# Optimization experiments

Measured on AMD Instinct MI355X. Metric: run time of the kernel, lower is better.

The kernel has to match this reference:

```python
import jax, jax.numpy as jnp
import numpy as np

D_MODEL = 1024


def setup_inputs() -> dict:
    key = jax.random.key(0)
    kx, kq, kk, kv = jax.random.split(key, 4)
    x = jax.random.normal(kx, (4, 2048, D_MODEL), dtype=jnp.float32)
    s = 1.0 / np.sqrt(D_MODEL)
    # torch nn.Linear weight is [out, in]; y = x @ W.T
    Wq = jax.random.normal(kq, (D_MODEL, D_MODEL), dtype=jnp.float32) * s
    Wk = jax.random.normal(kk, (D_MODEL, D_MODEL), dtype=jnp.float32) * s
    Wv = jax.random.normal(kv, (D_MODEL, D_MODEL), dtype=jnp.float32) * s
    return {"x": x, "Wq": Wq, "Wk": Wk, "Wv": Wv}


def reference(x, Wq, Wk, Wv):
    # Linear projections (no bias): [b, s, d]
    Q = jnp.einsum("bsd,ed->bse", x, Wq)
    K = jnp.einsum("bsd,ed->bse", x, Wk)
    V = jnp.einsum("bsd,ed->bse", x, Wv)
    d_k = Q.shape[-1]
    scores = jnp.einsum("bqd,bkd->bqk", Q, K) / jnp.sqrt(jnp.asarray(d_k, Q.dtype))
    weights = jax.nn.softmax(scores, axis=-1)
    return jnp.einsum("bqk,bkd->bqd", weights, V)
```

## Files before the change

### kernel.cpp

```cpp
#include <hip/hip_runtime.h>
#include <hip/hip_bf16.h>

using bf16 = __hip_bfloat16;
typedef __attribute__((ext_vector_type(8))) short short8;
typedef __attribute__((ext_vector_type(4))) float f32x4;

__global__ __launch_bounds__(256) void cast_f32_to_bf16(const float* __restrict__ in,
                                                        bf16* __restrict__ out) {
  const int i = (blockIdx.x * 256 + threadIdx.x) * 4;
  const float4 f = *(const float4*)(in + i);
  bf16 h[4];
  h[0] = __float2bfloat16(f.x);
  h[1] = __float2bfloat16(f.y);
  h[2] = __float2bfloat16(f.z);
  h[3] = __float2bfloat16(f.w);
  *(uint2*)(out + i) = *(const uint2*)h;
}

template <class Epi>
__device__ __forceinline__ void gemm128_nt(const bf16* __restrict__ A, const bf16* __restrict__ B,
                                           int lda, int ldb, int K, Epi epi) {
  __shared__ char smem[36864];
  bf16* As = (bf16*)smem;
  bf16* Bs = (bf16*)(smem + 8192);
  const int t = threadIdx.x;
  const int lane = t & 63;
  const int wave = t >> 6;
  const int wm = (wave >> 1) * 64;
  const int wn = (wave & 1) * 64;
  const int m0 = blockIdx.y * 128;
  const int n0 = blockIdx.x * 128;

  f32x4 acc[4][4];
#pragma unroll
  for (int i = 0; i < 4; ++i)
#pragma unroll
    for (int j = 0; j < 4; ++j)
#pragma unroll
      for (int r = 0; r < 4; ++r) acc[i][j][r] = 0.f;

  const int r0 = t >> 2;
  const int fsw = (r0 + (r0 >> 2)) & 3;
  const int cglob = ((t & 3) ^ fsw) << 3;
  const bf16* gA0 = A + (size_t)(m0 + r0) * lda + cglob;
  const bf16* gB0 = B + (size_t)(n0 + r0) * ldb + cglob;
  const bf16* gA1 = gA0 + (size_t)64 * lda;
  const bf16* gB1 = gB0 + (size_t)64 * ldb;
  bf16* lA = As + (size_t)wave * 64 * 8;
  bf16* lB = Bs + (size_t)wave * 64 * 8;

  const int fr = lane & 15;
  const int ffr = (fr + (fr >> 2)) & 3;
  const int csw = ((lane >> 4) ^ ffr) << 3;

  for (int k0 = 0; k0 < K; k0 += 32) {
    __builtin_amdgcn_global_load_lds((const __attribute__((address_space(1))) unsigned int*)(gA0 + k0),
                                     (__attribute__((address_space(3))) unsigned int*)lA, 16, 0, 0);
    __builtin_amdgcn_global_load_lds((const __attribute__((address_space(1))) unsigned int*)(gB0 + k0),
                                     (__attribute__((address_space(3))) unsigned int*)lB, 16, 0, 0);
    __builtin_amdgcn_global_load_lds((const __attribute__((address_space(1))) unsigned int*)(gA1 + k0),
                                     (__attribute__((address_space(3))) unsigned int*)(lA + 2048), 16, 0, 0);
    __builtin_amdgcn_global_load_lds((const __attribute__((address_space(1))) unsigned int*)(gB1 + k0),
                                     (__attribute__((address_space(3))) unsigned int*)(lB + 2048), 16, 0, 0);
    __syncthreads();

    short8 af[4], bfr[4];
#pragma unroll
    for (int mt = 0; mt < 4; ++mt)
      af[mt] = *(const short8*)(As + (wm + mt * 16 + fr) * 32 + csw);
#pragma unroll
    for (int nt = 0; nt < 4; ++nt)
      bfr[nt] = *(const short8*)(Bs + (wn + nt * 16 + fr) * 32 + csw);
#pragma unroll
    for (int mt = 0; mt < 4; ++mt)
#pragma unroll
      for (int nt = 0; nt < 4; ++nt)
        acc[mt][nt] = __builtin_amdgcn_mfma_f32_16x16x32_bf16(af[mt], bfr[nt], acc[mt][nt], 0, 0, 0);
    __syncthreads();
  }

  epi(acc, m0, n0, wm, wn, lane, wave, smem);
}

template <class F>
__device__ __forceinline__ void for_each_c(const f32x4 (&acc)[4][4], int m0, int n0, int wm,
                                           int wn, int lane, F f) {
  const int cr = (lane >> 4) * 4;
  const int cc = lane & 15;
#pragma unroll
  for (int mt = 0; mt < 4; ++mt)
#pragma unroll
    for (int nt = 0; nt < 4; ++nt)
#pragma unroll
      for (int r = 0; r < 4; ++r)
        f(m0 + wm + mt * 16 + cr + r, n0 + wn + nt * 16 + cc, acc[mt][nt][r]);
}

__global__ __launch_bounds__(256) void proj_kernel(const bf16* __restrict__ xb,
                                                   const bf16* __restrict__ Wb,
                                                   bf16* __restrict__ Qb, bf16* __restrict__ Kb,
                                                   bf16* __restrict__ Vt) {
  gemm128_nt(xb, Wb, 1024, 1024, 1024,
             [=](const f32x4 (&acc)[4][4], int m0, int n0, int wm, int wn, int lane, int wave,
                 char* smem) {
    if (n0 < 2048) {
      bf16* dst = (n0 < 1024) ? Qb : Kb;
      const int nb = (n0 < 1024) ? n0 : (n0 - 1024);
      for_each_c(acc, m0, nb, wm, wn, lane, [&](int m, int n, float v) {
        dst[(size_t)m * 1024 + n] = __float2bfloat16(v);
      });
    } else {
      bf16* T = (bf16*)smem + wave * 4608;
      const int cr = (lane >> 4) * 4;
      const int cc = lane & 15;
#pragma unroll
      for (int mt = 0; mt < 4; ++mt)
#pragma unroll
        for (int nt = 0; nt < 4; ++nt) {
          bf16 h4[4];
#pragma unroll
          for (int r = 0; r < 4; ++r) h4[r] = __float2bfloat16(acc[mt][nt][r]);
          *(uint2*)(T + (nt * 16 + cc) * 72 + mt * 16 + cr) = *(const uint2*)h4;
        }
      asm volatile("s_waitcnt lgkmcnt(0)" ::: "memory");
      const int mbase = m0 + wm;
      const int bb = mbase >> 11;
      const int sbase = mbase & 2047;
      const int nvbase = n0 - 2048 + wn;
#pragma unroll
      for (int i = 0; i < 8; ++i) {
        const int nl = i * 8 + (lane >> 3);
        const int ml = (lane & 7) * 8;
        const short8 val = *(const short8*)(T + nl * 72 + ml);
        *(short8*)(Vt + ((size_t)bb * 1024 + nvbase + nl) * 2048 + sbase + ml) = val;
      }
    }
  });
}

__global__ __launch_bounds__(256) void qk_exp_kernel(const bf16* __restrict__ Qb,
                                                     const bf16* __restrict__ Kb,
                                                     bf16* __restrict__ E,
                                                     float* __restrict__ Lpart) {
  const int z = blockIdx.z;
  const bf16* A = Qb + (size_t)z * 2048 * 1024;
  const bf16* B = Kb + (size_t)z * 2048 * 1024;
  bf16* Ez = E + (size_t)z * 2048 * 2048;
  float* Lz = Lpart + (size_t)z * 16 * 2048;
  gemm128_nt(A, B, 1024, 1024, 1024,
             [=](const f32x4 (&acc)[4][4], int m0, int n0, int wm, int wn, int lane, int wave,
                 char* smem) {
    float* Lp = (float*)smem;
    const int cr = (lane >> 4) * 4;
    const int cc = lane & 15;
#pragma unroll
    for (int mt = 0; mt < 4; ++mt)
#pragma unroll
      for (int r = 0; r < 4; ++r) {
        const int mr = wm + mt * 16 + cr + r;
        float s = 0.f;
#pragma unroll
        for (int nt = 0; nt < 4; ++nt) {
          const float e = __expf(acc[mt][nt][r] * 0.03125f);
          Ez[(size_t)(m0 + mr) * 2048 + n0 + wn + nt * 16 + cc] = __float2bfloat16(e);
          s += e;
        }
        s += __shfl_xor(s, 1, 64);
        s += __shfl_xor(s, 2, 64);
        s += __shfl_xor(s, 4, 64);
        s += __shfl_xor(s, 8, 64);
        if (cc == 0) Lp[mr * 2 + (wave & 1)] = s;
      }
    __syncthreads();
    const int t = threadIdx.x;
    if (t < 128) Lz[(n0 >> 7) * 2048 + m0 + t] = Lp[t * 2 + 0] + Lp[t * 2 + 1];
  });
}

__global__ __launch_bounds__(256) void reduce_l_kernel(const float* __restrict__ Lpart,
                                                       float* __restrict__ invL) {
  const int i = blockIdx.x * 256 + threadIdx.x;
  const int z = i >> 11, m = i & 2047;
  const float* p = Lpart + (size_t)z * 16 * 2048 + m;
  float s = 0.f;
#pragma unroll
  for (int t = 0; t < 16; ++t) s += p[(size_t)t * 2048];
  invL[i] = 1.f / s;
}

__global__ __launch_bounds__(256) void pv_kernel(const bf16* __restrict__ E,
                                                 const bf16* __restrict__ Vt,
                                                 const float* __restrict__ invL,
                                                 float* __restrict__ out) {
  const int z = blockIdx.z;
  const bf16* A = E + (size_t)z * 2048 * 2048;
  const bf16* B = Vt + (size_t)z * 1024 * 2048;
  const float* ilz = invL + (size_t)z * 2048;
  float* oz = out + (size_t)z * 2048 * 1024;
  gemm128_nt(A, B, 2048, 2048, 2048,
             [=](const f32x4 (&acc)[4][4], int m0, int n0, int wm, int wn, int lane, int wave,
                 char* smem) {
    const int cr = (lane >> 4) * 4;
    const int cc = lane & 15;
#pragma unroll
    for (int mt = 0; mt < 4; ++mt)
#pragma unroll
      for (int r = 0; r < 4; ++r) {
        const int m = m0 + wm + mt * 16 + cr + r;
        const float il = ilz[m];
#pragma unroll
        for (int nt = 0; nt < 4; ++nt)
          oz[(size_t)m * 1024 + n0 + wn + nt * 16 + cc] = acc[mt][nt][r] * il;
      }
  });
}

extern "C" void kernel_launch(void* const* d_in, const int* in_sizes, int n_in,
                              void* d_out, int out_size, void* d_ws, size_t ws_size,
                              hipStream_t stream) {
  const float* x = (const float*)d_in[0];
  const float* Wq = (const float*)d_in[1];
  const float* Wk = (const float*)d_in[2];
  const float* Wv = (const float*)d_in[3];
  float* out = (float*)d_out;

  char* w = (char*)d_ws;
  bf16* xb = (bf16*)w; w += (size_t)8192 * 1024 * 2;
  bf16* Wb = (bf16*)w; w += (size_t)3072 * 1024 * 2;
  bf16* Qb = (bf16*)w; w += (size_t)8192 * 1024 * 2;
  bf16* Kb = (bf16*)w; w += (size_t)8192 * 1024 * 2;
  bf16* Vt = (bf16*)w; w += (size_t)8192 * 1024 * 2;
  bf16* E  = (bf16*)w; w += (size_t)4 * 2048 * 2048 * 2;
  float* Lpart = (float*)w; w += (size_t)4 * 16 * 2048 * 4;
  float* invL  = (float*)w; w += (size_t)4 * 2048 * 4;

  cast_f32_to_bf16<<<8192, 256, 0, stream>>>(x, xb);
  cast_f32_to_bf16<<<1024, 256, 0, stream>>>(Wq, Wb);
  cast_f32_to_bf16<<<1024, 256, 0, stream>>>(Wk, Wb + (size_t)1024 * 1024);
  cast_f32_to_bf16<<<1024, 256, 0, stream>>>(Wv, Wb + (size_t)2048 * 1024);

  proj_kernel<<<dim3(24, 64), 256, 0, stream>>>(xb, Wb, Qb, Kb, Vt);

  qk_exp_kernel<<<dim3(16, 16, 4), 256, 0, stream>>>(Qb, Kb, E, Lpart);
  reduce_l_kernel<<<32, 256, 0, stream>>>(Lpart, invL);

  pv_kernel<<<dim3(8, 16, 4), 256, 0, stream>>>(E, Vt, invL, out);
}
```

Before: 268.6 us.

## Switch GEMM core to 32x32x16 MFMA tiles and merge weight casts

Replaces the 16x16x32 bf16 MFMA tiling (4x4 tiles per wave) with 32x32x16 MFMA (2x2 tiles per wave, two k-substeps per 32-wide LDS tile), and rewrites every epilogue's C-fragment indexing for the new accumulator layout. Each operand fragment now feeds a larger MFMA, so fewer LDS reads are needed per unit of math. The three weight-cast launches are merged into one kernel to cut launch overhead. The epilogue store patterns change: rows are strided by 8 and columns span 32 lanes, which shifts global write coalescing.

```diff
diff --git a/kernel.cpp b/kernel.cpp
--- a/kernel.cpp
+++ b/kernel.cpp
@@ -3,7 +3,7 @@
 
 using bf16 = __hip_bfloat16;
 typedef __attribute__((ext_vector_type(8))) short short8;
-typedef __attribute__((ext_vector_type(4))) float f32x4;
+typedef __attribute__((ext_vector_type(16))) float f32x16;
 
 __global__ __launch_bounds__(256) void cast_f32_to_bf16(const float* __restrict__ in,
                                                         bf16* __restrict__ out) {
@@ -15,6 +15,24 @@
   h[2] = __float2bfloat16(f.z);
   h[3] = __float2bfloat16(f.w);
   *(uint2*)(out + i) = *(const uint2*)h;
+}
+
+__global__ __launch_bounds__(256) void cast_weights(const float* __restrict__ Wq,
+                                                    const float* __restrict__ Wk,
+                                                    const float* __restrict__ Wv,
+                                                    bf16* __restrict__ out) {
+  const int b = blockIdx.x;
+  const float* src = (b < 1024) ? (Wq + (size_t)b * 1024)
+                   : (b < 2048) ? (Wk + (size_t)(b - 1024) * 1024)
+                                : (Wv + (size_t)(b - 2048) * 1024);
+  const int i = threadIdx.x * 4;
+  const float4 f = *(const float4*)(src + i);
+  bf16 h[4];
+  h[0] = __float2bfloat16(f.x);
+  h[1] = __float2bfloat16(f.y);
+  h[2] = __float2bfloat16(f.z);
+  h[3] = __float2bfloat16(f.w);
+  *(uint2*)(out + (size_t)b * 1024 + i) = *(const uint2*)h;
 }
 
 template <class Epi>
@@ -31,13 +49,13 @@
   const int m0 = blockIdx.y * 128;
   const int n0 = blockIdx.x * 128;
 
-  f32x4 acc[4][4];
-#pragma unroll
-  for (int i = 0; i < 4; ++i)
-#pragma unroll
-    for (int j = 0; j < 4; ++j)
-#pragma unroll
-      for (int r = 0; r < 4; ++r) acc[i][j][r] = 0.f;
+  f32x16 acc[2][2];
+#pragma unroll
+  for (int i = 0; i < 2; ++i)
+#pragma unroll
+    for (int j = 0; j < 2; ++j)
+#pragma unroll
+      for (int r = 0; r < 16; ++r) acc[i][j][r] = 0.f;
 
   const int r0 = t >> 2;
   const int fsw = (r0 + (r0 >> 2)) & 3;
@@ -49,9 +67,9 @@
   bf16* lA = As + (size_t)wave * 64 * 8;
   bf16* lB = Bs + (size_t)wave * 64 * 8;
 
-  const int fr = lane & 15;
-  const int ffr = (fr + (fr >> 2)) & 3;
-  const int csw = ((lane >> 4) ^ ffr) << 3;
+  const int rl = lane & 31;
+  const int grp = lane >> 5;
+  const int ffr = (rl + (rl >> 2)) & 3;
 
   for (int k0 = 0; k0 < K; k0 += 32) {
     __builtin_amdgcn_global_load_lds((const __attribute__((address_space(1))) unsigned int*)(gA0 + k0),
@@ -64,36 +82,47 @@
                                      (__attribute__((address_space(3))) unsigned int*)(lB + 2048), 16, 0, 0);
     __syncthreads();
 
-    short8 af[4], bfr[4];
-#pragma unroll
-    for (int mt = 0; mt < 4; ++mt)
-      af[mt] = *(const short8*)(As + (wm + mt * 16 + fr) * 32 + csw);
-#pragma unroll
-    for (int nt = 0; nt < 4; ++nt)
-      bfr[nt] = *(const short8*)(Bs + (wn + nt * 16 + fr) * 32 + csw);
-#pragma unroll
-    for (int mt = 0; mt < 4; ++mt)
-#pragma unroll
-      for (int nt = 0; nt < 4; ++nt)
-        acc[mt][nt] = __builtin_amdgcn_mfma_f32_16x16x32_bf16(af[mt], bfr[nt], acc[mt][nt], 0, 0, 0);
+    short8 af[2][2], bfr[2][2];
+#pragma unroll
+    for (int ks = 0; ks < 2; ++ks) {
+      const int kb = ks * 2 + grp;
+      const int co = ((kb ^ ffr) << 3);
+#pragma unroll
+      for (int mt = 0; mt < 2; ++mt)
+        af[ks][mt] = *(const short8*)(As + (wm + mt * 32 + rl) * 32 + co);
+#pragma unroll
+      for (int nt = 0; nt < 2; ++nt)
+        bfr[ks][nt] = *(const short8*)(Bs + (wn + nt * 32 + rl) * 32 + co);
+    }
+#pragma unroll
+    for (int ks = 0; ks < 2; ++ks)
+#pragma unroll
+      for (int mt = 0; mt < 2; ++mt)
+#pragma unroll
+        for (int nt = 0; nt < 2; ++nt)
+          acc[mt][nt] = __builtin_amdgcn_mfma_f32_32x32x16_bf16(af[ks][mt], bfr[ks][nt],
+                                                                acc[mt][nt], 0, 0, 0);
     __syncthreads();
   }
 
   epi(acc, m0, n0, wm, wn, lane, wave, smem);
 }
 
+__device__ __forceinline__ int c_row(int reg, int lane) {
+  return (reg & 3) + 8 * (reg >> 2) + 4 * (lane >> 5);
+}
+
 template <class F>
-__device__ __forceinline__ void for_each_c(const f32x4 (&acc)[4][4], int m0, int n0, int wm,
+__device__ __forceinline__ void for_each_c(const f32x16 (&acc)[2][2], int m0, int n0, int wm,
                                            int wn, int lane, F f) {
-  const int cr = (lane >> 4) * 4;
-  const int cc = lane & 15;
-#pragma unroll
-  for (int mt = 0; mt < 4; ++mt)
-#pragma unroll
-    for (int nt = 0; nt < 4; ++nt)
-#pragma unroll
-      for (int r = 0; r < 4; ++r)
-        f(m0 + wm + mt * 16 + cr + r, n0 + wn + nt * 16 + cc, acc[mt][nt][r]);
+  const int rl = lane & 31;
+#pragma unroll
+  for (int mt = 0; mt < 2; ++mt)
+#pragma unroll
+    for (int nt = 0; nt < 2; ++nt)
+#pragma unroll
+      for (int reg = 0; reg < 16; ++reg)
+        f(m0 + wm + mt * 32 + c_row(reg, lane), n0 + wn + nt * 32 + rl, acc[mt][nt][reg]);
 }
 
 __global__ __launch_bounds__(256) void proj_kernel(const bf16* __restrict__ xb,
@@ -101,7 +130,7 @@
                                                    bf16* __restrict__ Qb, bf16* __restrict__ Kb,
                                                    bf16* __restrict__ Vt) {
   gemm128_nt(xb, Wb, 1024, 1024, 1024,
-             [=](const f32x4 (&acc)[4][4], int m0, int n0, int wm, int wn, int lane, int wave,
+             [=](const f32x16 (&acc)[2][2], int m0, int n0, int wm, int wn, int lane, int wave,
                  char* smem) {
     if (n0 < 2048) {
       bf16* dst = (n0 < 1024) ? Qb : Kb;
@@ -111,17 +140,19 @@
       });
     } else {
       bf16* T = (bf16*)smem + wave * 4608;
-      const int cr = (lane >> 4) * 4;
-      const int cc = lane & 15;
-#pragma unroll
-      for (int mt = 0; mt < 4; ++mt)
-#pragma unroll
-        for (int nt = 0; nt < 4; ++nt) {
-          bf16 h4[4];
-#pragma unroll
-          for (int r = 0; r < 4; ++r) h4[r] = __float2bfloat16(acc[mt][nt][r]);
-          *(uint2*)(T + (nt * 16 + cc) * 72 + mt * 16 + cr) = *(const uint2*)h4;
-        }
+      const int rl = lane & 31;
+      const int g4 = 4 * (lane >> 5);
+#pragma unroll
+      for (int mt = 0; mt < 2; ++mt)
+#pragma unroll
+        for (int nt = 0; nt < 2; ++nt)
+#pragma unroll
+          for (int q = 0; q < 4; ++q) {
+            bf16 h4[4];
+#pragma unroll
+            for (int r = 0; r < 4; ++r) h4[r] = __float2bfloat16(acc[mt][nt][4 * q + r]);
+            *(uint2*)(T + (nt * 32 + rl) * 72 + mt * 32 + 8 * q + g4) = *(const uint2*)h4;
+          }
       asm volatile("s_waitcnt lgkmcnt(0)" ::: "memory");
       const int mbase = m0 + wm;
       const int bb = mbase >> 11;
@@ -148,28 +179,28 @@
   bf16* Ez = E + (size_t)z * 2048 * 2048;
   float* Lz = Lpart + (size_t)z * 16 * 2048;
   gemm128_nt(A, B, 1024, 1024, 1024,
-             [=](const f32x4 (&acc)[4][4], int m0, int n0, int wm, int wn, int lane, int wave,
+             [=](const f32x16 (&acc)[2][2], int m0, int n0, int wm, int wn, int lane, int wave,
                  char* smem) {
     float* Lp = (float*)smem;
-    const int cr = (lane >> 4) * 4;
-    const int cc = lane & 15;
-#pragma unroll
-    for (int mt = 0; mt < 4; ++mt)
-#pragma unroll
-      for (int r = 0; r < 4; ++r) {
-        const int mr = wm + mt * 16 + cr + r;
+    const int rl = lane & 31;
+#pragma unroll
+    for (int mt = 0; mt < 2; ++mt)
+#pragma unroll
+      for (int reg = 0; reg < 16; ++reg) {
+        const int mr = wm + mt * 32 + c_row(reg, lane);
         float s = 0.f;
 #pragma unroll
-        for (int nt = 0; nt < 4; ++nt) {
-          const float e = __expf(acc[mt][nt][r] * 0.03125f);
-          Ez[(size_t)(m0 + mr) * 2048 + n0 + wn + nt * 16 + cc] = __float2bfloat16(e);
+        for (int nt = 0; nt < 2; ++nt) {
+          const float e = __expf(acc[mt][nt][reg] * 0.03125f);
+          Ez[(size_t)(m0 + mr) * 2048 + n0 + wn + nt * 32 + rl] = __float2bfloat16(e);
           s += e;
         }
         s += __shfl_xor(s, 1, 64);
         s += __shfl_xor(s, 2, 64);
         s += __shfl_xor(s, 4, 64);
         s += __shfl_xor(s, 8, 64);
-        if (cc == 0) Lp[mr * 2 + (wave & 1)] = s;
+        s += __shfl_xor(s, 16, 64);
+        if (rl == 0) Lp[mr * 2 + (wave & 1)] = s;
       }
     __syncthreads();
     const int t = threadIdx.x;
@@ -198,19 +229,18 @@
   const float* ilz = invL + (size_t)z * 2048;
   float* oz = out + (size_t)z * 2048 * 1024;
   gemm128_nt(A, B, 2048, 2048, 2048,
-             [=](const f32x4 (&acc)[4][4], int m0, int n0, int wm, int wn, int lane, int wave,
+             [=](const f32x16 (&acc)[2][2], int m0, int n0, int wm, int wn, int lane, int wave,
                  char* smem) {
-    const int cr = (lane >> 4) * 4;
-    const int cc = lane & 15;
-#pragma unroll
-    for (int mt = 0; mt < 4; ++mt)
-#pragma unroll
-      for (int r = 0; r < 4; ++r) {
-        const int m = m0 + wm + mt * 16 + cr + r;
+    const int rl = lane & 31;
+#pragma unroll
+    for (int mt = 0; mt < 2; ++mt)
+#pragma unroll
+      for (int reg = 0; reg < 16; ++reg) {
+        const int m = m0 + wm + mt * 32 + c_row(reg, lane);
         const float il = ilz[m];
 #pragma unroll
-        for (int nt = 0; nt < 4; ++nt)
-          oz[(size_t)m * 1024 + n0 + wn + nt * 16 + cc] = acc[mt][nt][r] * il;
+        for (int nt = 0; nt < 2; ++nt)
+          oz[(size_t)m * 1024 + n0 + wn + nt * 32 + rl] = acc[mt][nt][reg] * il;
       }
   });
 }
@@ -235,9 +265,7 @@
   float* invL  = (float*)w; w += (size_t)4 * 2048 * 4;
 
   cast_f32_to_bf16<<<8192, 256, 0, stream>>>(x, xb);
-  cast_f32_to_bf16<<<1024, 256, 0, stream>>>(Wq, Wb);
-  cast_f32_to_bf16<<<1024, 256, 0, stream>>>(Wk, Wb + (size_t)1024 * 1024);
-  cast_f32_to_bf16<<<1024, 256, 0, stream>>>(Wv, Wb + (size_t)2048 * 1024);
+  cast_weights<<<3072, 256, 0, stream>>>(Wq, Wk, Wv, Wb);
 
   proj_kernel<<<dim3(24, 64), 256, 0, stream>>>(xb, Wb, Qb, Kb, Vt);
 
```

New measurement: 265.4 us. Within noise of the previous version (-1.2%).
